# Performance work log

Measured on AMD Instinct MI355X. Metric: run time of the kernel, lower is better.

The kernel has to match this reference:

```python
import jax, jax.numpy as jnp
import numpy as np

N, IN_F, H, F = 4096, 256, 8, 64
NEG_INF = -1e9  # stand-in for -inf; avoids NaNs for fully-masked rows


def setup_inputs() -> dict:
    key = jax.random.key(0)
    k1, k2, k3, k4, k5 = jax.random.split(key, 5)
    h = jax.random.normal(k1, (N, IN_F), dtype=jnp.float32)
    adj = jax.random.randint(k2, (N, N), 0, 2, dtype=jnp.int32)
    # xavier-ish scaled params
    W = jax.random.normal(k3, (IN_F, H * F), dtype=jnp.float32) * (2.0 / (IN_F + H * F)) ** 0.5
    a_src = jax.random.normal(k4, (H, F), dtype=jnp.float32) * (2.0 / (H * F)) ** 0.5
    a_dst = jax.random.normal(k5, (H, F), dtype=jnp.float32) * (2.0 / (H * F)) ** 0.5
    bias = jnp.zeros((H * F,), dtype=jnp.float32)
    return {"h": h, "adj": adj, "W": W, "a_src": a_src, "a_dst": a_dst, "bias": bias}


def reference(h, adj, W, a_src, a_dst, bias):
    # Wh: [N, H, F]
    Wh = (h @ W).reshape(N, H, F)
    e_src = jnp.einsum('nhf,hf->nh', Wh, a_src)  # [N, H]
    e_dst = jnp.einsum('nhf,hf->nh', Wh, a_dst)  # [N, H]
    e = e_src[:, None, :] + e_dst[None, :, :]    # [N, N, H]
    e = jnp.where(e > 0, e, 0.2 * e)             # LeakyReLU(0.2)
    e = jnp.where((adj != 0)[:, :, None], e, NEG_INF)
    alpha = jax.nn.softmax(e, axis=1)            # softmax over neighbors j
    # h_prime[i,h,f] = sum_j alpha[i,j,h] * Wh[j,h,f]
    h_prime = jnp.einsum('ijh,jhf->ihf', alpha, Wh)
    h_prime = h_prime.reshape(N, H * F)          # concat=True
    return h_prime + bias
```

## Files before the change

### kernel.cpp

```cpp
#include <hip/hip_runtime.h>
#include <stdint.h>

#define NN   4096
#define KIN  256
#define NH   8
#define FD   64
#define HFD  512
#define BI   16
#define JT   64
#define NTILES (NN / JT)

typedef __attribute__((ext_vector_type(4))) float  floatx4;
typedef __attribute__((ext_vector_type(8))) short  short8;

__device__ __forceinline__ unsigned short f2bf_rne(float x) {
    uint32_t u = __float_as_uint(x);
    u += 0x7FFFu + ((u >> 16) & 1u);
    return (unsigned short)(u >> 16);
}
__device__ __forceinline__ float bf2f(unsigned short b) {
    return __uint_as_float(((uint32_t)b) << 16);
}
__device__ __forceinline__ uint32_t packtrunc(float lo, float hi) {
    return (__float_as_uint(hi) & 0xFFFF0000u) | (__float_as_uint(lo) >> 16);
}
__device__ __forceinline__ uint32_t bit2mask(uint32_t b, int n) {
    return (((b >> (2 * n)) & 1u) ? 0x0000FFFFu : 0u) |
           (((b >> (2 * n + 1)) & 1u) ? 0xFFFF0000u : 0u);
}

__global__ __launch_bounds__(256) void k0_prep(
        const float* __restrict__ hmat, const float* __restrict__ Wmat,
        const int* __restrict__ adj,
        unsigned short* __restrict__ h_hi, unsigned short* __restrict__ h_lo,
        unsigned short* __restrict__ wt_hi, unsigned short* __restrict__ wt_lo,
        uint32_t* __restrict__ bm) {
    const int bx = blockIdx.x, tid = threadIdx.x;
    if (bx < 1024) {
        const int e0 = (bx * 256 + tid) * 4;
        const float4 v = *reinterpret_cast<const float4*>(&hmat[e0]);
        ushort4 hi, lo;
        hi.x = f2bf_rne(v.x); lo.x = f2bf_rne(v.x - bf2f(hi.x));
        hi.y = f2bf_rne(v.y); lo.y = f2bf_rne(v.y - bf2f(hi.y));
        hi.z = f2bf_rne(v.z); lo.z = f2bf_rne(v.z - bf2f(hi.z));
        hi.w = f2bf_rne(v.w); lo.w = f2bf_rne(v.w - bf2f(hi.w));
        *reinterpret_cast<ushort4*>(&h_hi[e0]) = hi;
        *reinterpret_cast<ushort4*>(&h_lo[e0]) = lo;
    } else if (bx < 1536) {
        const int c = bx - 1024;
        const float v = Wmat[(size_t)tid * HFD + c];
        const unsigned short hi = f2bf_rne(v);
        const unsigned short lo = f2bf_rne(v - bf2f(hi));
        wt_hi[c * KIN + tid] = hi;
        wt_lo[c * KIN + tid] = lo;
    } else {
        const int widx = (bx - 1536) * 256 + tid;
        const size_t base = (size_t)widx * 32;
        uint32_t m = 0;
        #pragma unroll
        for (int u = 0; u < 8; ++u) {
            const int4 a = *reinterpret_cast<const int4*>(&adj[base + u * 4]);
            m |= (a.x ? 1u : 0u) << (u * 4 + 0);
            m |= (a.y ? 1u : 0u) << (u * 4 + 1);
            m |= (a.z ? 1u : 0u) << (u * 4 + 2);
            m |= (a.w ? 1u : 0u) << (u * 4 + 3);
        }
        bm[widx] = m;
    }
}

__global__ __launch_bounds__(256) void k1_front(
        const unsigned short* __restrict__ h_hi, const unsigned short* __restrict__ h_lo,
        const unsigned short* __restrict__ wt_hi, const unsigned short* __restrict__ wt_lo,
        const float* __restrict__ a_src, const float* __restrict__ a_dst,
        unsigned short* __restrict__ whbT,
        float* __restrict__ esrcT, float* __restrict__ edstT) {
    const int tid  = threadIdx.x;
    const int w    = tid >> 6;
    const int lane = tid & 63;
    const int g = lane >> 4, lr = lane & 15;
    const int n0  = blockIdx.x * 64;
    const int hd  = blockIdx.y;
    const int hf0 = hd * FD;
    const int row = n0 + w * 16 + lr;
    floatx4 acc[4] = {};
    #pragma unroll
    for (int k0 = 0; k0 < KIN; k0 += 32) {
        const short8 ahi = *reinterpret_cast<const short8*>(&h_hi[(size_t)row * KIN + k0 + g * 8]);
        const short8 alo = *reinterpret_cast<const short8*>(&h_lo[(size_t)row * KIN + k0 + g * 8]);
        #pragma unroll
        for (int ni = 0; ni < 4; ++ni) {
            const size_t bo = (size_t)(hf0 + ni * 16 + lr) * KIN + k0 + g * 8;
            const short8 bhi = *reinterpret_cast<const short8*>(&wt_hi[bo]);
            const short8 blo = *reinterpret_cast<const short8*>(&wt_lo[bo]);
            acc[ni] = __builtin_amdgcn_mfma_f32_16x16x32_bf16(ahi, bhi, acc[ni], 0, 0, 0);
            acc[ni] = __builtin_amdgcn_mfma_f32_16x16x32_bf16(ahi, blo, acc[ni], 0, 0, 0);
            acc[ni] = __builtin_amdgcn_mfma_f32_16x16x32_bf16(alo, bhi, acc[ni], 0, 0, 0);
        }
    }
    #pragma unroll
    for (int ni = 0; ni < 4; ++ni) {
        const int hf = hf0 + ni * 16 + lr;
        ushort4 o;
        o.x = f2bf_rne(acc[ni][0]); o.y = f2bf_rne(acc[ni][1]);
        o.z = f2bf_rne(acc[ni][2]); o.w = f2bf_rne(acc[ni][3]);
        *reinterpret_cast<ushort4*>(&whbT[(size_t)hf * NN + n0 + w * 16 + g * 4]) = o;
    }
    float asv[4], adv[4];
    #pragma unroll
    for (int ni = 0; ni < 4; ++ni) {
        asv[ni] = a_src[hf0 + ni * 16 + lr];
        adv[ni] = a_dst[hf0 + ni * 16 + lr];
    }
    #pragma unroll
    for (int r = 0; r < 4; ++r) {
        float ps = 0.f, pd = 0.f;
        #pragma unroll
        for (int ni = 0; ni < 4; ++ni) { ps += acc[ni][r] * asv[ni]; pd += acc[ni][r] * adv[ni]; }
        #pragma unroll
        for (int off = 1; off < 16; off <<= 1) {
            ps += __shfl_xor(ps, off, 64);
            pd += __shfl_xor(pd, off, 64);
        }
        if (lr == 0) {
            esrcT[hd * NN + n0 + w * 16 + g * 4 + r] = ps;
            edstT[hd * NN + n0 + w * 16 + g * 4 + r] = pd;
        }
    }
}

__global__ __launch_bounds__(256) void k2_tables(
        const float* __restrict__ esrcT, const float* __restrict__ edstT,
        float* __restrict__ es1T, float* __restrict__ es2T,
        float* __restrict__ ed1T, float* __restrict__ ed2T) {
    __shared__ float red[256];
    const int hd = blockIdx.x, tid = threadIdx.x;
    float m = -1e30f;
    for (int n = tid; n < NN; n += 256) m = fmaxf(m, edstT[hd * NN + n]);
    red[tid] = m;
    __syncthreads();
    for (int s = 128; s > 0; s >>= 1) {
        if (tid < s) red[tid] = fmaxf(red[tid], red[tid + s]);
        __syncthreads();
    }
    const float maxd = red[0];
    for (int n = tid; n < NN; n += 256) {
        const float ed = edstT[hd * NN + n];
        ed1T[hd * NN + n] = __expf(ed);
        ed2T[hd * NN + n] = __expf(0.2f * ed);
        const float es = esrcT[hd * NN + n];
        const float t  = es + maxd;
        const float M  = fmaxf(t, 0.2f * t);
        es1T[hd * NN + n] = __expf(es - M);
        es2T[hd * NN + n] = __expf(0.2f * es - M);
    }
}

__global__ __launch_bounds__(256) void k3_attn(
        const uint32_t* __restrict__ bm, const unsigned short* __restrict__ whbT,
        const float* __restrict__ es1T, const float* __restrict__ es2T,
        const float* __restrict__ ed1T, const float* __restrict__ ed2T,
        const float* __restrict__ bias, float* __restrict__ out) {
    __shared__ uint32_t bmLds[BI * 129];
    const int tid  = threadIdx.x;
    const int lane = tid & 63;
    const int wl   = tid >> 6;
    const int bx   = blockIdx.x;
    const int iblk = bx >> 1;
    const int hgrp = bx & 1;
    const int head = hgrp * 4 + wl;
    const int hf0  = head * FD;
    const int i0   = iblk * BI;
    const int g  = lane >> 4;
    const int lr = lane & 15;
    const int jrot = (bx & 7) * 512;

    #pragma unroll
    for (int u = 0; u < 8; ++u) {
        const int idx = u * 256 + tid;
        const int r = idx >> 7, w = idx & 127;
        bmLds[r * 129 + w] = bm[(size_t)(i0 + r) * 128 + w];
    }
    __syncthreads();

    const float es1 = es1T[head * NN + i0 + lr];
    const float es2 = es2T[head * NN + i0 + lr];
    float bs[4];
    #pragma unroll
    for (int ni = 0; ni < 4; ++ni) bs[ni] = bias[hf0 + ni * 16 + lr];

    floatx4 acc[4] = {};
    floatx4 accd = {};
    short8 ones;
    #pragma unroll
    for (int e = 0; e < 8; ++e) ones[e] = (short)0x3F80;

    const int wbase = lr * 129;
    for (int t = 0; t < NTILES; ++t) {
        const int j0 = (jrot + t * JT) & (NN - 1);
        const int wi = j0 >> 5;
        const uint32_t w0 = bmLds[wbase + wi];
        const uint32_t w1 = bmLds[wbase + wi + 1];

        short8 bfrag[2][4];
        #pragma unroll
        for (int ks = 0; ks < 2; ++ks)
            #pragma unroll
            for (int ni = 0; ni < 4; ++ni)
                bfrag[ks][ni] = *reinterpret_cast<const short8*>(
                    &whbT[(size_t)(hf0 + ni * 16 + lr) * NN + j0 + ks * 32 + g * 8]);

        #pragma unroll
        for (int ks = 0; ks < 2; ++ks) {
            const uint32_t b = ((ks ? w1 : w0) >> (g * 8)) & 0xFFu;
            const int jo = head * NN + j0 + ks * 32 + g * 8;
            const float4 e1a = *reinterpret_cast<const float4*>(&ed1T[jo]);
            const float4 e1b = *reinterpret_cast<const float4*>(&ed1T[jo + 4]);
            const float4 e2a = *reinterpret_cast<const float4*>(&ed2T[jo]);
            const float4 e2b = *reinterpret_cast<const float4*>(&ed2T[jo + 4]);
            union { uint32_t wd[4]; short8 s8; } pu;
            pu.wd[0] = packtrunc(fmaxf(es1 * e1a.x, es2 * e2a.x),
                                 fmaxf(es1 * e1a.y, es2 * e2a.y)) & bit2mask(b, 0);
            pu.wd[1] = packtrunc(fmaxf(es1 * e1a.z, es2 * e2a.z),
                                 fmaxf(es1 * e1a.w, es2 * e2a.w)) & bit2mask(b, 1);
            pu.wd[2] = packtrunc(fmaxf(es1 * e1b.x, es2 * e2b.x),
                                 fmaxf(es1 * e1b.y, es2 * e2b.y)) & bit2mask(b, 2);
            pu.wd[3] = packtrunc(fmaxf(es1 * e1b.z, es2 * e2b.z),
                                 fmaxf(es1 * e1b.w, es2 * e2b.w)) & bit2mask(b, 3);
            #pragma unroll
            for (int ni = 0; ni < 4; ++ni)
                acc[ni] = __builtin_amdgcn_mfma_f32_16x16x32_bf16(
                    pu.s8, bfrag[ks][ni], acc[ni], 0, 0, 0);
            accd = __builtin_amdgcn_mfma_f32_16x16x32_bf16(pu.s8, ones, accd, 0, 0, 0);
        }
    }

    float inv[4];
    #pragma unroll
    for (int r = 0; r < 4; ++r) inv[r] = 1.0f / accd[r];
    #pragma unroll
    for (int ni = 0; ni < 4; ++ni)
        #pragma unroll
        for (int r = 0; r < 4; ++r)
            out[(size_t)(i0 + g * 4 + r) * HFD + hf0 + ni * 16 + lr] =
                acc[ni][r] * inv[r] + bs[ni];
}

extern "C" void kernel_launch(void* const* d_in, const int* in_sizes, int n_in,
                              void* d_out, int out_size, void* d_ws, size_t ws_size,
                              hipStream_t stream) {
    const float* hmat  = (const float*)d_in[0];
    const int*   adj   = (const int*)d_in[1];
    const float* Wmat  = (const float*)d_in[2];
    const float* a_src = (const float*)d_in[3];
    const float* a_dst = (const float*)d_in[4];
    const float* bias  = (const float*)d_in[5];
    float* out = (float*)d_out;

    char* ws = (char*)d_ws;
    unsigned short* whbT = (unsigned short*)ws;
    float* esrcT = (float*)(ws + (4u << 20));
    float* edstT = esrcT + NH * NN;
    float* es1T  = edstT + NH * NN;
    float* es2T  = es1T + NH * NN;
    float* ed1T  = es2T + NH * NN;
    float* ed2T  = ed1T + NH * NN;
    uint32_t* bmk = (uint32_t*)(ed2T + NH * NN);
    unsigned short* h_hi = (unsigned short*)(bmk + (NN / 32) * NN);
    unsigned short* h_lo = h_hi + (size_t)NN * KIN;
    unsigned short* wt_hi = h_lo + (size_t)NN * KIN;
    unsigned short* wt_lo = wt_hi + (size_t)KIN * HFD;

    k0_prep<<<dim3(3584), 256, 0, stream>>>(hmat, Wmat, adj, h_hi, h_lo, wt_hi, wt_lo, bmk);
    k1_front<<<dim3(64, 8), 256, 0, stream>>>(h_hi, h_lo, wt_hi, wt_lo, a_src, a_dst,
                                              whbT, esrcT, edstT);
    k2_tables<<<dim3(NH), 256, 0, stream>>>(esrcT, edstT, es1T, es2T, ed1T, ed2T);
    k3_attn<<<dim3(512), 256, 0, stream>>>(bmk, whbT, es1T, es2T, ed1T, ed2T, bias, out);
}
```

Baseline: 282.5 us.

## Split attention j-range across blocks with partial sums, double-buffer loads, add reduce kernel

```diff
diff --git a/kernel.cpp b/kernel.cpp
--- a/kernel.cpp
+++ b/kernel.cpp
@@ -8,7 +8,9 @@
 #define HFD  512
 #define BI   16
 #define JT   64
-#define NTILES (NN / JT)
+#define NC2  2
+#define CH   (NN / NC2)
+#define NT2  (CH / JT)
 
 typedef __attribute__((ext_vector_type(4))) float  floatx4;
 typedef __attribute__((ext_vector_type(8))) short  short8;
@@ -156,38 +158,40 @@
     }
 }
 
-__global__ __launch_bounds__(256) void k3_attn(
+__global__ __launch_bounds__(256, 4) void k3_attn(
         const uint32_t* __restrict__ bm, const unsigned short* __restrict__ whbT,
         const float* __restrict__ es1T, const float* __restrict__ es2T,
         const float* __restrict__ ed1T, const float* __restrict__ ed2T,
-        const float* __restrict__ bias, float* __restrict__ out) {
-    __shared__ uint32_t bmLds[BI * 129];
+        float* __restrict__ numP, float* __restrict__ denP) {
+    __shared__ uint32_t bmLds[BI * 65];
     const int tid  = threadIdx.x;
     const int lane = tid & 63;
     const int wl   = tid >> 6;
     const int bx   = blockIdx.x;
-    const int iblk = bx >> 1;
-    const int hgrp = bx & 1;
+    const int xcd  = bx & 7;
+    const int r8   = bx >> 3;
+    const int jc   = xcd >> 2;
+    const int l4   = xcd & 3;
+    const int hgrp = r8 & 1;
+    const int iblk = (r8 >> 1) + 64 * l4;
     const int head = hgrp * 4 + wl;
     const int hf0  = head * FD;
     const int i0   = iblk * BI;
     const int g  = lane >> 4;
     const int lr = lane & 15;
-    const int jrot = (bx & 7) * 512;
-
-    #pragma unroll
-    for (int u = 0; u < 8; ++u) {
+    const int jbase = jc * CH;
+    const int jrot  = l4 * 512;
+
+    #pragma unroll
+    for (int u = 0; u < 4; ++u) {
         const int idx = u * 256 + tid;
-        const int r = idx >> 7, w = idx & 127;
-        bmLds[r * 129 + w] = bm[(size_t)(i0 + r) * 128 + w];
+        const int rr = idx >> 6, w = idx & 63;
+        bmLds[rr * 65 + w] = bm[(size_t)(i0 + rr) * 128 + jc * 64 + w];
     }
     __syncthreads();
 
     const float es1 = es1T[head * NN + i0 + lr];
     const float es2 = es2T[head * NN + i0 + lr];
-    float bs[4];
-    #pragma unroll
-    for (int ni = 0; ni < 4; ++ni) bs[ni] = bias[hf0 + ni * 16 + lr];
 
     floatx4 acc[4] = {};
     floatx4 accd = {};
@@ -195,24 +199,25 @@
     #pragma unroll
     for (int e = 0; e < 8; ++e) ones[e] = (short)0x3F80;
 
-    const int wbase = lr * 129;
-    for (int t = 0; t < NTILES; ++t) {
-        const int j0 = (jrot + t * JT) & (NN - 1);
-        const int wi = j0 >> 5;
-        const uint32_t w0 = bmLds[wbase + wi];
-        const uint32_t w1 = bmLds[wbase + wi + 1];
-
-        short8 bfrag[2][4];
+    auto LD = [&](int t, short8 (&bf)[2][4], uint32_t &m0, uint32_t &m1) {
+        const int jl = (jrot + t * JT) & (CH - 1);
+        const int j0 = jbase + jl;
         #pragma unroll
         for (int ks = 0; ks < 2; ++ks)
             #pragma unroll
             for (int ni = 0; ni < 4; ++ni)
-                bfrag[ks][ni] = *reinterpret_cast<const short8*>(
+                bf[ks][ni] = *reinterpret_cast<const short8*>(
                     &whbT[(size_t)(hf0 + ni * 16 + lr) * NN + j0 + ks * 32 + g * 8]);
-
+        const int wi = jl >> 5;
+        m0 = bmLds[lr * 65 + wi];
+        m1 = bmLds[lr * 65 + wi + 1];
+    };
+    auto CP = [&](int t, short8 (&bf)[2][4], uint32_t m0, uint32_t m1) {
+        const int jl = (jrot + t * JT) & (CH - 1);
+        const int j0 = jbase + jl;
         #pragma unroll
         for (int ks = 0; ks < 2; ++ks) {
-            const uint32_t b = ((ks ? w1 : w0) >> (g * 8)) & 0xFFu;
+            const uint32_t b = ((ks ? m1 : m0) >> (g * 8)) & 0xFFu;
             const int jo = head * NN + j0 + ks * 32 + g * 8;
             const float4 e1a = *reinterpret_cast<const float4*>(&ed1T[jo]);
             const float4 e1b = *reinterpret_cast<const float4*>(&ed1T[jo + 4]);
@@ -230,20 +235,56 @@
             #pragma unroll
             for (int ni = 0; ni < 4; ++ni)
                 acc[ni] = __builtin_amdgcn_mfma_f32_16x16x32_bf16(
-                    pu.s8, bfrag[ks][ni], acc[ni], 0, 0, 0);
+                    pu.s8, bf[ks][ni], acc[ni], 0, 0, 0);
             accd = __builtin_amdgcn_mfma_f32_16x16x32_bf16(pu.s8, ones, accd, 0, 0, 0);
         }
-    }
-
-    float inv[4];
-    #pragma unroll
-    for (int r = 0; r < 4; ++r) inv[r] = 1.0f / accd[r];
+    };
+
+    short8 bfA[2][4], bfB[2][4];
+    uint32_t mA0, mA1, mB0, mB1;
+    LD(0, bfA, mA0, mA1);
+    for (int t = 0; t < NT2; t += 2) {
+        LD(t + 1, bfB, mB0, mB1);
+        CP(t, bfA, mA0, mA1);
+        if (t + 2 < NT2) LD(t + 2, bfA, mA0, mA1);
+        CP(t + 1, bfB, mB0, mB1);
+    }
+
     #pragma unroll
     for (int ni = 0; ni < 4; ++ni)
         #pragma unroll
         for (int r = 0; r < 4; ++r)
-            out[(size_t)(i0 + g * 4 + r) * HFD + hf0 + ni * 16 + lr] =
-                acc[ni][r] * inv[r] + bs[ni];
+            numP[((size_t)jc * NN + i0 + g * 4 + r) * HFD + hf0 + ni * 16 + lr] =
+                acc[ni][r];
+    if (lr == 0) {
+        #pragma unroll
+        for (int r = 0; r < 4; ++r)
+            denP[((size_t)jc * NH + head) * NN + i0 + g * 4 + r] = accd[r];
+    }
+}
+
+__global__ __launch_bounds__(256) void k4_reduce(
+        const float* __restrict__ numP, const float* __restrict__ denP,
+        const float* __restrict__ bias, float* __restrict__ out) {
+    const int idx = blockIdx.x * 256 + threadIdx.x;
+    const int e0 = idx * 4;
+    const int i  = e0 >> 9;
+    const int hf = e0 & 511;
+    const int hd = hf >> 6;
+    float4 s = make_float4(0.f, 0.f, 0.f, 0.f);
+    float d = 0.f;
+    #pragma unroll
+    for (int c = 0; c < NC2; ++c) {
+        const float4 v = *reinterpret_cast<const float4*>(&numP[((size_t)c * NN + i) * HFD + hf]);
+        s.x += v.x; s.y += v.y; s.z += v.z; s.w += v.w;
+        d += denP[((size_t)c * NH + hd) * NN + i];
+    }
+    const float inv = 1.0f / d;
+    const float4 b = *reinterpret_cast<const float4*>(&bias[hf]);
+    float4 o;
+    o.x = s.x * inv + b.x; o.y = s.y * inv + b.y;
+    o.z = s.z * inv + b.z; o.w = s.w * inv + b.w;
+    *reinterpret_cast<float4*>(&out[(size_t)i * HFD + hf]) = o;
 }
 
 extern "C" void kernel_launch(void* const* d_in, const int* in_sizes, int n_in,
@@ -266,7 +307,9 @@
     float* ed1T  = es2T + NH * NN;
     float* ed2T  = ed1T + NH * NN;
     uint32_t* bmk = (uint32_t*)(ed2T + NH * NN);
-    unsigned short* h_hi = (unsigned short*)(bmk + (NN / 32) * NN);
+    float* numP = (float*)(bmk + (size_t)(NN / 32) * NN);
+    float* denP = numP + (size_t)NC2 * NN * HFD;
+    unsigned short* h_hi = (unsigned short*)numP;
     unsigned short* h_lo = h_hi + (size_t)NN * KIN;
     unsigned short* wt_hi = h_lo + (size_t)NN * KIN;
     unsigned short* wt_lo = wt_hi + (size_t)KIN * HFD;
@@ -275,5 +318,6 @@
     k1_front<<<dim3(64, 8), 256, 0, stream>>>(h_hi, h_lo, wt_hi, wt_lo, a_src, a_dst,
                                               whbT, esrcT, edstT);
     k2_tables<<<dim3(NH), 256, 0, stream>>>(esrcT, edstT, es1T, es2T, ed1T, ed2T);
-    k3_attn<<<dim3(512), 256, 0, stream>>>(bmk, whbT, es1T, es2T, ed1T, ed2T, bias, out);
-}
+    k3_attn<<<dim3(1024), 256, 0, stream>>>(bmk, whbT, es1T, es2T, ed1T, ed2T, numP, denP);
+    k4_reduce<<<dim3((NN * HFD / 4) / 256), 256, 0, stream>>>(numP, denP, bias, out);
+}
```

New measurement: 289.9 us. 2.6% more time.
